# Kernel optimization log

Measured on AMD Instinct MI355X. Metric: run time of the kernel, lower is better.

The kernel has to match this reference:

```python
import jax, jax.numpy as jnp
import numpy as np

T = 4096  # input sequence length; H = T - 16 after convs+pool


def setup_inputs() -> dict:
    key = jax.random.key(0)
    ks = jax.random.split(key, 20)
    def rn(k, shape, scale=0.05):
        return jax.random.normal(k, shape, dtype=jnp.float32) * scale
    return dict(
        evaluation=rn(ks[0], (T, 128), 1.0),
        template=rn(ks[1], (T, 128), 1.0),
        conv1_w=rn(ks[2], (16, 1, 5, 5)),  conv1_b=rn(ks[3], (16,)),
        conv2_w=rn(ks[4], (32, 16, 5, 5)), conv2_b=rn(ks[5], (32,)),
        conv3_w=rn(ks[6], (64, 32, 5, 5)), conv3_b=rn(ks[7], (64,)),
        lin1_w=rn(ks[8], (64, 3712)),      lin1_b=rn(ks[9], (64,)),
        gru_wih=rn(ks[10], (192, 64)),     gru_whh=rn(ks[11], (192, 64)),
        gru_bih=rn(ks[12], (192,)),        gru_bhh=rn(ks[13], (192,)),
        attn_w=rn(ks[14], (1, 64)),        attn_b=rn(ks[15], (1,)),
        lin3_w=rn(ks[16], (128, 64)),      lin3_b=rn(ks[17], (128,)),
        cls_w=rn(ks[18], (2, 128)),        cls_b=rn(ks[19], (2,)),
    )


def _conv(x, w, b):
    y = jax.lax.conv_general_dilated(x, w, (1, 1), 'VALID',
                                     dimension_numbers=('NCHW', 'OIHW', 'NCHW'))
    return y + b[None, :, None, None]


def _encode(x, c1w, c1b, c2w, c2b, c3w, c3b, l1w, l1b, wih, whh, bih, bhh):
    # x: (T, 128) -> (1, 1, T, 128); no activations between convs (as in source)
    x = x.reshape(1, 1, T, 128)
    x = _conv(x, c1w, c1b)   # (1,16,T-4,124)
    x = _conv(x, c2w, c2b)   # (1,32,T-8,120)
    x = _conv(x, c3w, c3b)   # (1,64,T-12,116)
    x = jax.lax.reduce_window(x, -jnp.inf, jax.lax.max,
                              (1, 1, 5, 2), (1, 1, 1, 2), 'VALID')  # (1,64,H,58)
    H = x.shape[2]
    # faithful raw reshape (channel-major flatten), same as torch.reshape
    x = x.reshape(H, 3712)
    x = x @ l1w.T + l1b      # (H, 64)
    # GRU (torch gate order r,z,n), h0 = 0; input gates precomputed
    gi = x @ wih.T + bih     # (H, 192)
    def step(h, gi_t):
        gh = whh @ h + bhh
        ir, iz, inn = jnp.split(gi_t, 3)
        hr, hz, hn = jnp.split(gh, 3)
        r = jax.nn.sigmoid(ir + hr)
        z = jax.nn.sigmoid(iz + hz)
        n = jnp.tanh(inn + r * hn)
        h_new = (1.0 - z) * n + z * h
        return h_new, h_new
    _, out = jax.lax.scan(step, jnp.zeros((64,), dtype=x.dtype), gi)
    return out               # (H, 64)


def reference(evaluation, template, conv1_w, conv1_b, conv2_w, conv2_b,
              conv3_w, conv3_b, lin1_w, lin1_b, gru_wih, gru_whh, gru_bih,
              gru_bhh, attn_w, attn_b, lin3_w, lin3_b, cls_w, cls_b):
    enc = lambda x: _encode(x, conv1_w, conv1_b, conv2_w, conv2_b, conv3_w,
                            conv3_b, lin1_w, lin1_b, gru_wih, gru_whh,
                            gru_bih, gru_bhh)
    e = enc(evaluation)      # (H, 64)
    t = enc(template)        # (H, 64)
    # alignment: aw[m,n] = <e_m, t_n>, softmax over dim 0 (m)
    aw = jax.nn.softmax(e @ t.T, axis=0)      # (H, H)
    t_prim = aw @ t                            # (H, 64)
    distance = jnp.abs(t_prim - e)             # (H, 64)
    attn = jax.nn.softmax((e @ attn_w.T + attn_b).ravel(), axis=0)  # (H,)
    # NOTE: source loops n over distance.size(dim=1)==64, i.e. only the first
    # 64 rows of distance / first 64 attention weights are used (replicated).
    D = distance.shape[1]
    representation = distance[:D].T @ attn[:D]  # (64,)
    out = jax.nn.relu(representation)
    out = jax.nn.relu(out @ lin3_w.T + lin3_b)
    return out @ cls_w.T + cls_b               # (2,)
```

## Files before the change

### kernel.cpp

```cpp
#include <hip/hip_runtime.h>
#include <hip/hip_fp16.h>

constexpr int T_IN = 4096, W_IN = 128;
constexpr int H1 = 4092, W1 = 124, C1 = 16;
constexpr int H2 = 4088, W2 = 120, C2 = 32;
constexpr int H3 = 4084, W3 = 116, C3 = 64;
constexpr int HP = 4080, WPW = 58;
constexpr int KF = 3712;

typedef float f32x16 __attribute__((ext_vector_type(16)));
typedef _Float16 f16x16 __attribute__((ext_vector_type(16)));
typedef _Float16 half2_t __attribute__((ext_vector_type(2)));

static __device__ __forceinline__ half2_t u2h(unsigned int u) {
    half2_t h; __builtin_memcpy(&h, &u, 4); return h;
}

#define LOAD25(SRC, W) \
    float p00=(SRC)[0],        p01=(SRC)[1],        p02=(SRC)[2],        p03=(SRC)[3],        p04=(SRC)[4]; \
    float p10=(SRC)[(W)],      p11=(SRC)[(W)+1],    p12=(SRC)[(W)+2],    p13=(SRC)[(W)+3],    p14=(SRC)[(W)+4]; \
    float p20=(SRC)[2*(W)],    p21=(SRC)[2*(W)+1],  p22=(SRC)[2*(W)+2],  p23=(SRC)[2*(W)+3],  p24=(SRC)[2*(W)+4]; \
    float p30=(SRC)[3*(W)],    p31=(SRC)[3*(W)+1],  p32=(SRC)[3*(W)+2],  p33=(SRC)[3*(W)+3],  p34=(SRC)[3*(W)+4]; \
    float p40=(SRC)[4*(W)],    p41=(SRC)[4*(W)+1],  p42=(SRC)[4*(W)+2],  p43=(SRC)[4*(W)+3],  p44=(SRC)[4*(W)+4];

#define TAPS25(T) \
    T(p00, 0)  T(p01, 1)  T(p02, 2)  T(p03, 3)  T(p04, 4) \
    T(p10, 5)  T(p11, 6)  T(p12, 7)  T(p13, 8)  T(p14, 9) \
    T(p20,10)  T(p21,11)  T(p22,12)  T(p23,13)  T(p24,14) \
    T(p30,15)  T(p31,16)  T(p32,17)  T(p33,18)  T(p34,19) \
    T(p40,20)  T(p41,21)  T(p42,22)  T(p43,23)  T(p44,24)

#define KSTEP16(PK, WPTR) do { \
    const float4* w4_ = (const float4*)(WPTR); \
    float4 wA_ = w4_[0], wB_ = w4_[1], wC_ = w4_[2], wD_ = w4_[3]; \
    a0.x = fmaf((PK), wA_.x, a0.x); a0.y = fmaf((PK), wA_.y, a0.y); \
    a0.z = fmaf((PK), wA_.z, a0.z); a0.w = fmaf((PK), wA_.w, a0.w); \
    a1.x = fmaf((PK), wB_.x, a1.x); a1.y = fmaf((PK), wB_.y, a1.y); \
    a1.z = fmaf((PK), wB_.z, a1.z); a1.w = fmaf((PK), wB_.w, a1.w); \
    a2.x = fmaf((PK), wC_.x, a2.x); a2.y = fmaf((PK), wC_.y, a2.y); \
    a2.z = fmaf((PK), wC_.z, a2.z); a2.w = fmaf((PK), wC_.w, a2.w); \
    a3.x = fmaf((PK), wD_.x, a3.x); a3.y = fmaf((PK), wD_.y, a3.y); \
    a3.z = fmaf((PK), wD_.z, a3.z); a3.w = fmaf((PK), wD_.w, a3.w); \
} while (0)

#define LOAD25H(SRC, W) \
    _Float16 q00=(_Float16)(SRC)[0],      q01=(_Float16)(SRC)[1],      q02=(_Float16)(SRC)[2],      q03=(_Float16)(SRC)[3],      q04=(_Float16)(SRC)[4]; \
    _Float16 q10=(_Float16)(SRC)[(W)],    q11=(_Float16)(SRC)[(W)+1],  q12=(_Float16)(SRC)[(W)+2],  q13=(_Float16)(SRC)[(W)+3],  q14=(_Float16)(SRC)[(W)+4]; \
    _Float16 q20=(_Float16)(SRC)[2*(W)],  q21=(_Float16)(SRC)[2*(W)+1],q22=(_Float16)(SRC)[2*(W)+2],q23=(_Float16)(SRC)[2*(W)+3],q24=(_Float16)(SRC)[2*(W)+4]; \
    _Float16 q30=(_Float16)(SRC)[3*(W)],  q31=(_Float16)(SRC)[3*(W)+1],q32=(_Float16)(SRC)[3*(W)+2],q33=(_Float16)(SRC)[3*(W)+3],q34=(_Float16)(SRC)[3*(W)+4]; \
    _Float16 q40=(_Float16)(SRC)[4*(W)],  q41=(_Float16)(SRC)[4*(W)+1],q42=(_Float16)(SRC)[4*(W)+2],q43=(_Float16)(SRC)[4*(W)+3],q44=(_Float16)(SRC)[4*(W)+4];

#define MKPAIRS() \
    half2_t P0, P1, P2, P3, P4, P5, P6, P7, P8, P9, P10, P11, P12; \
    P0[0]=q00; P0[1]=q01;  P1[0]=q02; P1[1]=q03;  P2[0]=q04; P2[1]=q10; \
    P3[0]=q11; P3[1]=q12;  P4[0]=q13; P4[1]=q14;  P5[0]=q20; P5[1]=q21; \
    P6[0]=q22; P6[1]=q23;  P7[0]=q24; P7[1]=q30;  P8[0]=q31; P8[1]=q32; \
    P9[0]=q33; P9[1]=q34;  P10[0]=q40; P10[1]=q41; P11[0]=q42; P11[1]=q43; \
    P12[0]=q44; P12[1]=(_Float16)0.f;

#define DSTEP16(PH, WPTR) do { \
    const half2_t* wv_ = (const half2_t*)(WPTR); \
    a0.x = __builtin_amdgcn_fdot2((PH), wv_[0],  a0.x, false); \
    a0.y = __builtin_amdgcn_fdot2((PH), wv_[1],  a0.y, false); \
    a0.z = __builtin_amdgcn_fdot2((PH), wv_[2],  a0.z, false); \
    a0.w = __builtin_amdgcn_fdot2((PH), wv_[3],  a0.w, false); \
    a1.x = __builtin_amdgcn_fdot2((PH), wv_[4],  a1.x, false); \
    a1.y = __builtin_amdgcn_fdot2((PH), wv_[5],  a1.y, false); \
    a1.z = __builtin_amdgcn_fdot2((PH), wv_[6],  a1.z, false); \
    a1.w = __builtin_amdgcn_fdot2((PH), wv_[7],  a1.w, false); \
    a2.x = __builtin_amdgcn_fdot2((PH), wv_[8],  a2.x, false); \
    a2.y = __builtin_amdgcn_fdot2((PH), wv_[9],  a2.y, false); \
    a2.z = __builtin_amdgcn_fdot2((PH), wv_[10], a2.z, false); \
    a2.w = __builtin_amdgcn_fdot2((PH), wv_[11], a2.w, false); \
    a3.x = __builtin_amdgcn_fdot2((PH), wv_[12], a3.x, false); \
    a3.y = __builtin_amdgcn_fdot2((PH), wv_[13], a3.y, false); \
    a3.z = __builtin_amdgcn_fdot2((PH), wv_[14], a3.z, false); \
    a3.w = __builtin_amdgcn_fdot2((PH), wv_[15], a3.w, false); \
} while (0)

#define PAIRS13(D, CI) \
    D(P0,  ((CI)*13+ 0)) D(P1,  ((CI)*13+ 1)) D(P2,  ((CI)*13+ 2)) \
    D(P3,  ((CI)*13+ 3)) D(P4,  ((CI)*13+ 4)) D(P5,  ((CI)*13+ 5)) \
    D(P6,  ((CI)*13+ 6)) D(P7,  ((CI)*13+ 7)) D(P8,  ((CI)*13+ 8)) \
    D(P9,  ((CI)*13+ 9)) D(P10, ((CI)*13+10)) D(P11, ((CI)*13+11)) \
    D(P12, ((CI)*13+12))

__global__ __launch_bounds__(256, 2) void conv1_k(const float* __restrict__ x,
        const float* __restrict__ wp, const float* __restrict__ b,
        __half* __restrict__ out) {
    int pos = blockIdx.x * 256 + threadIdx.x;
    if (pos >= H1 * W1) return;
    int h = pos / W1, wi = pos - h * W1;
    const float* src = x + h * W_IN + wi;
    const float4* b4 = (const float4*)b;
    float4 a0 = b4[0], a1 = b4[1], a2 = b4[2], a3 = b4[3];
    LOAD25(src, W_IN);
#define T1(P, K) KSTEP16(P, wp + (K) * 16);
    TAPS25(T1)
#undef T1
#pragma unroll
    for (int i = 0; i < 4; i++) {
        float4 v = (i == 0) ? a0 : (i == 1) ? a1 : (i == 2) ? a2 : a3;
        out[(size_t)(i * 4 + 0) * (H1 * W1) + pos] = __float2half(v.x);
        out[(size_t)(i * 4 + 1) * (H1 * W1) + pos] = __float2half(v.y);
        out[(size_t)(i * 4 + 2) * (H1 * W1) + pos] = __float2half(v.z);
        out[(size_t)(i * 4 + 3) * (H1 * W1) + pos] = __float2half(v.w);
    }
}

__global__ __launch_bounds__(256, 2) void conv2_k(const __half* __restrict__ in,
        const _Float16* __restrict__ wp2, const float* __restrict__ b,
        __half* __restrict__ out) {
    int pos = blockIdx.y * 256 + threadIdx.x;
    if (pos >= H2 * W2) return;
    int co0 = blockIdx.x * 16;
    int h = pos / W2, wi = pos - h * W2;
    const float4* b4 = (const float4*)(b + co0);
    float4 a0 = b4[0], a1 = b4[1], a2 = b4[2], a3 = b4[3];
#pragma unroll 1
    for (int ci = 0; ci < C1; ci++) {
        const __half* src = in + (size_t)ci * (H1 * W1) + h * W1 + wi;
        LOAD25H(src, W1);
        MKPAIRS();
#define D2(PH, QI) DSTEP16(PH, wp2 + ((size_t)(QI) * C2 + co0) * 2);
        PAIRS13(D2, ci)
#undef D2
    }
#pragma unroll
    for (int i = 0; i < 4; i++) {
        float4 v = (i == 0) ? a0 : (i == 1) ? a1 : (i == 2) ? a2 : a3;
        out[(size_t)(co0 + i * 4 + 0) * (H2 * W2) + pos] = __float2half(v.x);
        out[(size_t)(co0 + i * 4 + 1) * (H2 * W2) + pos] = __float2half(v.y);
        out[(size_t)(co0 + i * 4 + 2) * (H2 * W2) + pos] = __float2half(v.z);
        out[(size_t)(co0 + i * 4 + 3) * (H2 * W2) + pos] = __float2half(v.w);
    }
}

__global__ __launch_bounds__(256, 2) void conv3_k(const __half* __restrict__ in,
        const _Float16* __restrict__ wp2, const float* __restrict__ b,
        __half* __restrict__ out) {
    int pos = blockIdx.y * 256 + threadIdx.x;
    if (pos >= H3 * W3) return;
    int co0 = blockIdx.x * 16;
    int h = pos / W3, wi = pos - h * W3;
    const float4* b4 = (const float4*)(b + co0);
    float4 a0 = b4[0], a1 = b4[1], a2 = b4[2], a3 = b4[3];
#pragma unroll 1
    for (int ci = 0; ci < C2; ci++) {
        const __half* src = in + (size_t)ci * (H2 * W2) + h * W2 + wi;
        LOAD25H(src, W2);
        MKPAIRS();
#define D3(PH, QI) DSTEP16(PH, wp2 + ((size_t)(QI) * C3 + co0) * 2);
        PAIRS13(D3, ci)
#undef D3
    }
#pragma unroll
    for (int i = 0; i < 4; i++) {
        float4 v = (i == 0) ? a0 : (i == 1) ? a1 : (i == 2) ? a2 : a3;
        out[(size_t)(co0 + i * 4 + 0) * (H3 * W3) + pos] = __float2half(v.x);
        out[(size_t)(co0 + i * 4 + 1) * (H3 * W3) + pos] = __float2half(v.y);
        out[(size_t)(co0 + i * 4 + 2) * (H3 * W3) + pos] = __float2half(v.z);
        out[(size_t)(co0 + i * 4 + 3) * (H3 * W3) + pos] = __float2half(v.w);
    }
}

__global__ __launch_bounds__(256) void pool_k(const __half* __restrict__ in,
        _Float16* __restrict__ out) {
    int idx = blockIdx.x * 256 + threadIdx.x;
    if (idx >= C3 * HP * WPW) return;
    int w = idx % WPW; int rest = idx / WPW; int h = rest % HP; int c = rest / HP;
    const __half* base = in + (size_t)c * (H3 * W3) + (size_t)h * W3 + 2 * w;
    float m = -1e30f;
#pragma unroll
    for (int i = 0; i < 5; i++)
#pragma unroll
        for (int j = 0; j < 2; j++)
            m = fmaxf(m, __half2float(base[(size_t)i * W3 + j]));
    out[idx] = (_Float16)m;
}

__global__ __launch_bounds__(256, 2) void lin1_k(const _Float16* __restrict__ X,
        const _Float16* __restrict__ Wt2, float* __restrict__ L) {
    __shared__ unsigned int Xs[32][68];
    int tid = threadIdx.x;
    int j = tid & 63, mg = tid >> 6;
    int m0 = blockIdx.x * 64;
    int c0 = blockIdx.y * 15;
    int c1 = (c0 + 15 < 58) ? c0 + 15 : 58;
    float4 la0 = {0.f,0.f,0.f,0.f}, la1 = la0, la2 = la0, la3 = la0;
    for (int cc = c0; cc < c1; cc++) {
        int k0 = cc * 64, kp0 = cc * 32;
        __syncthreads();
#pragma unroll
        for (int t = 0; t < 8; t++) {
            int idx = tid + t * 256;
            int mm = idx >> 5, kk = idx & 31;
            int m = m0 + mm;
            unsigned int v = 0;
            if (m < HP) v = *(const unsigned int*)(X + (size_t)m * KF + k0 + 2 * kk);
            Xs[kk][mm] = v;
        }
        __syncthreads();
#pragma unroll 4
        for (int kk = 0; kk < 32; kk++) {
            unsigned int wvu = *(const unsigned int*)(Wt2 + ((size_t)(kp0 + kk) * 64 + j) * 2);
            half2_t wv = u2h(wvu);
            const uint4* xr = (const uint4*)&Xs[kk][mg * 16];
            uint4 x0 = xr[0], x1 = xr[1], x2 = xr[2], x3 = xr[3];
            la0.x = __builtin_amdgcn_fdot2(u2h(x0.x), wv, la0.x, false);
            la0.y = __builtin_amdgcn_fdot2(u2h(x0.y), wv, la0.y, false);
            la0.z = __builtin_amdgcn_fdot2(u2h(x0.z), wv, la0.z, false);
            la0.w = __builtin_amdgcn_fdot2(u2h(x0.w), wv, la0.w, false);
            la1.x = __builtin_amdgcn_fdot2(u2h(x1.x), wv, la1.x, false);
            la1.y = __builtin_amdgcn_fdot2(u2h(x1.y), wv, la1.y, false);
            la1.z = __builtin_amdgcn_fdot2(u2h(x1.z), wv, la1.z, false);
            la1.w = __builtin_amdgcn_fdot2(u2h(x1.w), wv, la1.w, false);
            la2.x = __builtin_amdgcn_fdot2(u2h(x2.x), wv, la2.x, false);
            la2.y = __builtin_amdgcn_fdot2(u2h(x2.y), wv, la2.y, false);
            la2.z = __builtin_amdgcn_fdot2(u2h(x2.z), wv, la2.z, false);
            la2.w = __builtin_amdgcn_fdot2(u2h(x2.w), wv, la2.w, false);
            la3.x = __builtin_amdgcn_fdot2(u2h(x3.x), wv, la3.x, false);
            la3.y = __builtin_amdgcn_fdot2(u2h(x3.y), wv, la3.y, false);
            la3.z = __builtin_amdgcn_fdot2(u2h(x3.z), wv, la3.z, false);
            la3.w = __builtin_amdgcn_fdot2(u2h(x3.w), wv, la3.w, false);
        }
    }
    int mb = m0 + mg * 16;
#define LATOM(C, OFF) { int m = mb + (OFF); if (m < HP) atomicAdd(&L[(size_t)m * 64 + j], (C)); }
    LATOM(la0.x, 0)  LATOM(la0.y, 1)  LATOM(la0.z, 2)  LATOM(la0.w, 3)
    LATOM(la1.x, 4)  LATOM(la1.y, 5)  LATOM(la1.z, 6)  LATOM(la1.w, 7)
    LATOM(la2.x, 8)  LATOM(la2.y, 9)  LATOM(la2.z, 10) LATOM(la2.w, 11)
    LATOM(la3.x, 12) LATOM(la3.y, 13) LATOM(la3.z, 14) LATOM(la3.w, 15)
#undef LATOM
}

__global__ __launch_bounds__(192) void gi_k(const float* __restrict__ L,
        const float* __restrict__ wiht, const float* __restrict__ bc,
        float* __restrict__ gi) {
    __shared__ alignas(16) float Ls[8][64];
    int m0 = blockIdx.x * 8, g = threadIdx.x;
    for (int idx = g; idx < 512; idx += 192) {
        int r = idx >> 6, k = idx & 63;
        Ls[r][k] = L[(size_t)(m0 + r) * 64 + k];
    }
    __syncthreads();
    float bcv = bc[g];
#pragma unroll 1
    for (int r = 0; r < 8; r++) {
        float acc = bcv;
#pragma unroll
        for (int k = 0; k < 64; k++) acc = fmaf(Ls[r][k], wiht[k * 192 + g], acc);
        gi[(size_t)(m0 + r) * 192 + g] = acc;
    }
}

__global__ __launch_bounds__(192, 1) void gru_k(const float* __restrict__ gi0,
        const float* __restrict__ gi1, const _Float16* __restrict__ whh_h,
        const float* __restrict__ bhh, float* __restrict__ e,
        float* __restrict__ t) {
    const float* gi = blockIdx.x ? gi1 : gi0;
    float* out = blockIdx.x ? t : e;
    const int g = threadIdx.x;
    const f16x16* wp = (const f16x16*)(whh_h + (size_t)g * 64);
    f16x16 w0 = wp[0], w1 = wp[1], w2 = wp[2], w3 = wp[3];
    float bh = bhh[g];
    __shared__ alignas(64) _Float16 hs[64];
    __shared__ float Ax[192];
    const f16x16* hsv = (const f16x16*)hs;
    float h = 0.f;
    if (g < 64) hs[g] = (_Float16)0.f;
    __syncthreads();
    float p0 = 0.f, p1 = 0.f, p2 = 0.f;
    if (g < 64) { p0 = gi[g]; p1 = gi[64 + g]; p2 = gi[128 + g]; }
#define LGKM_BARRIER() do { \
    asm volatile("s_waitcnt lgkmcnt(0)" ::: "memory"); \
    __builtin_amdgcn_s_barrier(); \
    asm volatile("" ::: "memory"); \
} while (0)
#define DOT8(W, H, ACC) _Pragma("unroll") \
    for (int i_ = 0; i_ < 8; i_++) { \
        half2_t wa_; wa_[0] = (W)[2*i_]; wa_[1] = (W)[2*i_+1]; \
        half2_t ha_; ha_[0] = (H)[2*i_]; ha_[1] = (H)[2*i_+1]; \
        ACC = __builtin_amdgcn_fdot2(wa_, ha_, ACC, false); \
    }
#pragma unroll 1
    for (int m = 0; m < HP; m++) {
        f16x16 hv0 = hsv[0], hv1 = hsv[1], hv2 = hsv[2], hv3 = hsv[3];
        float c0 = p0, c1 = p1, c2 = p2;
        if (g < 64 && m + 1 < HP) {
            const float* gp = gi + (size_t)(m + 1) * 192;
            p0 = gp[g]; p1 = gp[64 + g]; p2 = gp[128 + g];
        }
        float a0 = 0.f, a1 = 0.f, a2 = 0.f, a3 = 0.f;
        DOT8(w0, hv0, a0)
        DOT8(w1, hv1, a1)
        DOT8(w2, hv2, a2)
        DOT8(w3, hv3, a3)
        float a = (a0 + a1) + (a2 + a3) + bh;
        Ax[g] = a;
        LGKM_BARRIER();
        if (g < 64) {
            float az = Ax[64 + g], an = Ax[128 + g];
            float rg = 1.f / (1.f + __expf(-(c0 + a)));
            float zg = 1.f / (1.f + __expf(-(c1 + az)));
            float pre = c2 + rg * an;
            float ex = __expf(2.f * pre);
            float nn = 1.f - 2.f / (ex + 1.f);
            h = (1.f - zg) * nn + zg * h;
            hs[g] = (_Float16)h;
            out[(size_t)m * 64 + g] = h;
        }
        LGKM_BARRIER();
    }
#undef DOT8
#undef LGKM_BARRIER
}

__global__ __launch_bounds__(256) void astat_k(const float* __restrict__ e,
        const float* __restrict__ t, float* __restrict__ pM,
        float* __restrict__ pZ) {
    __shared__ alignas(16) float Ts[64][68];
    __shared__ float Ms[4][64], Zs[4][64];
    int tid = threadIdx.x;
    int nl = tid & 63, ms = tid >> 6;
    int n0 = blockIdx.x * 64;
#pragma unroll
    for (int i = 0; i < 16; i++) {
        int idx = tid + i * 256;
        int rr = idx >> 6, kk = idx & 63;
        int n = n0 + rr;
        Ts[rr][kk] = (n < HP) ? t[(size_t)n * 64 + kk] : 0.f;
    }
    __syncthreads();
    float M = -1e30f, Z = 0.f;
    int m0 = blockIdx.y * 510;
    const float4* Trow = (const float4*)&Ts[nl][0];
    for (int m = m0 + ms; m < m0 + 510; m += 4) {
        const float4* er = (const float4*)(e + (size_t)m * 64);
        float a0 = 0, a1 = 0, a2 = 0, a3 = 0;
#pragma unroll
        for (int i = 0; i < 16; i++) {
            float4 evv = er[i], tv = Trow[i];
            a0 = fmaf(evv.x, tv.x, a0); a1 = fmaf(evv.y, tv.y, a1);
            a2 = fmaf(evv.z, tv.z, a2); a3 = fmaf(evv.w, tv.w, a3);
        }
        float s = (a0 + a1) + (a2 + a3);
        float nM = fmaxf(M, s);
        Z = Z * __expf(M - nM) + __expf(s - nM);
        M = nM;
    }
    Ms[ms][nl] = M; Zs[ms][nl] = Z;
    __syncthreads();
    if (ms == 0) {
#pragma unroll
        for (int i = 1; i < 4; i++) {
            float m2 = Ms[i][nl], z2 = Zs[i][nl];
            float nM = fmaxf(M, m2);
            Z = Z * __expf(M - nM) + z2 * __expf(m2 - nM);
            M = nM;
        }
        int n = n0 + nl;
        if (n < HP) { pM[(size_t)blockIdx.y * HP + n] = M; pZ[(size_t)blockIdx.y * HP + n] = Z; }
    }
}

__global__ __launch_bounds__(256) void attnlog_k(const float* __restrict__ e,
        const float* __restrict__ aw, const float* __restrict__ ab,
        float* __restrict__ alog) {
    int m = blockIdx.x * 256 + threadIdx.x;
    if (m >= HP) return;
    float acc = ab[0];
    const float4* er = (const float4*)(e + (size_t)m * 64);
    const float4* ar = (const float4*)aw;
#pragma unroll
    for (int i = 0; i < 16; i++) {
        float4 evv = er[i], av = ar[i];
        acc += evv.x * av.x + evv.y * av.y + evv.z * av.z + evv.w * av.w;
    }
    alog[m] = acc;
}

__global__ __launch_bounds__(256) void reduce_k(const float* __restrict__ pM,
        const float* __restrict__ pZ, float* __restrict__ Mn,
        float* __restrict__ Zn, const float* __restrict__ alog,
        float* __restrict__ scal) {
    int tid = threadIdx.x;
    if (blockIdx.x < 16) {
        int n = blockIdx.x * 256 + tid;
        if (n >= HP) return;
        float M = pM[n], Z = pZ[n];
#pragma unroll
        for (int y = 1; y < 8; y++) {
            float m2 = pM[(size_t)y * HP + n], z2 = pZ[(size_t)y * HP + n];
            float nM = fmaxf(M, m2);
            Z = Z * __expf(M - nM) + z2 * __expf(m2 - nM);
            M = nM;
        }
        Mn[n] = M; Zn[n] = Z;
    } else {
        __shared__ float red[256];
        float m = -1e30f;
        for (int i = tid; i < HP; i += 256) m = fmaxf(m, alog[i]);
        red[tid] = m; __syncthreads();
        for (int s = 128; s > 0; s >>= 1) {
            if (tid < s) red[tid] = fmaxf(red[tid], red[tid + s]);
            __syncthreads();
        }
        float Ma = red[0]; __syncthreads();
        float z = 0.f;
        for (int i = tid; i < HP; i += 256) z += __expf(alog[i] - Ma);
        red[tid] = z; __syncthreads();
        for (int s = 128; s > 0; s >>= 1) {
            if (tid < s) red[tid] += red[tid + s];
            __syncthreads();
        }
        if (tid == 0) { scal[0] = Ma; scal[1] = red[0]; }
    }
}

__global__ __launch_bounds__(256) void wmat_k(const float* __restrict__ e,
        const float* __restrict__ t, const float* __restrict__ Mn,
        const float* __restrict__ Zn, float* __restrict__ Wm) {
    __shared__ alignas(16) float Es[64][68];
    int tid = threadIdx.x;
#pragma unroll
    for (int i = 0; i < 16; i++) {
        int idx = tid + i * 256;
        int rr = idx >> 6, kk = idx & 63;
        Es[rr][kk] = e[(size_t)rr * 64 + kk];
    }
    __syncthreads();
    int n = blockIdx.x * 256 + tid;
    if (n >= HP) return;
    float tn[64];
    const float4* tr = (const float4*)(t + (size_t)n * 64);
    float4* tn4 = (float4*)tn;
#pragma unroll
    for (int i = 0; i < 16; i++) tn4[i] = tr[i];
    float mM = Mn[n], iZ = 1.f / Zn[n];
#pragma unroll 1
    for (int m = 0; m < 64; m++) {
        const float4* Er = (const float4*)&Es[m][0];
        float a0 = 0, a1 = 0, a2 = 0, a3 = 0;
#pragma unroll
        for (int i = 0; i < 16; i++) {
            float4 evv = Er[i], tv = tn4[i];
            a0 = fmaf(evv.x, tv.x, a0); a1 = fmaf(evv.y, tv.y, a1);
            a2 = fmaf(evv.z, tv.z, a2); a3 = fmaf(evv.w, tv.w, a3);
        }
        float s = (a0 + a1) + (a2 + a3);
        Wm[(size_t)m * HP + n] = __expf(s - mM) * iZ;
    }
}

__global__ __launch_bounds__(256) void tprim_k(const float* __restrict__ Wm,
        const float* __restrict__ t, float* __restrict__ tp) {
    __shared__ float Ws[64][64];
    __shared__ float Ts[64][64];
    int tid = threadIdx.x;
    int n0 = blockIdx.x * 64;
#pragma unroll
    for (int i = 0; i < 16; i++) {
        int idx = tid + i * 256;
        int r = idx >> 6, c = idx & 63;
        Ws[r][c] = (n0 + c < HP) ? Wm[(size_t)r * HP + n0 + c] : 0.f;
        Ts[r][c] = (n0 + r < HP) ? t[(size_t)(n0 + r) * 64 + c] : 0.f;
    }
    __syncthreads();
    int d = tid & 63, mg = tid >> 6;
    float acc[16];
#pragma unroll
    for (int i = 0; i < 16; i++) acc[i] = 0.f;
    for (int k = 0; k < 64; k++) {
        float tv = Ts[k][d];
#pragma unroll
        for (int mm = 0; mm < 16; mm++) acc[mm] = fmaf(Ws[mg * 16 + mm][k], tv, acc[mm]);
    }
#pragma unroll
    for (int mm = 0; mm < 16; mm++)
        atomicAdd(&tp[(size_t)(mg * 16 + mm) * 64 + d], acc[mm]);
}

__global__ __launch_bounds__(256) void final_k(const float* __restrict__ tp,
        const float* __restrict__ e, const float* __restrict__ alog,
        const float* __restrict__ scal, const float* __restrict__ l3w,
        const float* __restrict__ l3b, const float* __restrict__ cw,
        const float* __restrict__ cb, float* __restrict__ out) {
    __shared__ float r1[64], hid[128];
    int tid = threadIdx.x;
    float Ma = scal[0], iZa = 1.f / scal[1];
    if (tid < 64) {
        float acc = 0.f;
        for (int m = 0; m < 64; m++) {
            float a = __expf(alog[m] - Ma) * iZa;
            acc += fabsf(tp[m * 64 + tid] - e[m * 64 + tid]) * a;
        }
        r1[tid] = fmaxf(acc, 0.f);
    }
    __syncthreads();
    if (tid < 128) {
        float acc = l3b[tid];
        for (int d = 0; d < 64; d++) acc = fmaf(r1[d], l3w[tid * 64 + d], acc);
        hid[tid] = fmaxf(acc, 0.f);
    }
    __syncthreads();
    if (tid < 2) {
        float acc = cb[tid];
        for (int j = 0; j < 128; j++) acc = fmaf(hid[j], cw[tid * 128 + j], acc);
        out[tid] = acc;
    }
}

__global__ __launch_bounds__(256) void pack_l1w2_k(const float* __restrict__ w,
        _Float16* __restrict__ wt2) {
    int idx = blockIdx.x * 256 + threadIdx.x;
    if (idx >= (KF / 2) * 64) return;
    int kk = idx >> 6, j = idx & 63;
    wt2[(size_t)idx * 2 + 0] = (_Float16)w[(size_t)j * KF + 2 * kk];
    wt2[(size_t)idx * 2 + 1] = (_Float16)w[(size_t)j * KF + 2 * kk + 1];
}
__global__ __launch_bounds__(256) void pack_w1_k(const float* __restrict__ w,
        float* __restrict__ wp) {
    int idx = blockIdx.x * 256 + threadIdx.x;
    if (idx >= 400) return;
    int k = idx >> 4, co = idx & 15;
    wp[idx] = w[co * 25 + k];
}
__global__ __launch_bounds__(256) void pack_w2p_k(const float* __restrict__ w,
        _Float16* __restrict__ wp2) {
    int idx = blockIdx.x * 256 + threadIdx.x;
    if (idx >= 16 * 13 * 32) return;
    int co = idx & 31; int rest = idx >> 5;
    int q = rest % 13, ci = rest / 13;
    int t0 = 2 * q, t1 = 2 * q + 1;
    float v0 = (t0 < 25) ? w[co * 400 + ci * 25 + t0] : 0.f;
    float v1 = (t1 < 25) ? w[co * 400 + ci * 25 + t1] : 0.f;
    wp2[(size_t)idx * 2 + 0] = (_Float16)v0;
    wp2[(size_t)idx * 2 + 1] = (_Float16)v1;
}
__global__ __launch_bounds__(256) void pack_w3p_k(const float* __restrict__ w,
        _Float16* __restrict__ wp2) {
    int idx = blockIdx.x * 256 + threadIdx.x;
    if (idx >= 32 * 13 * 64) return;
    int co = idx & 63; int rest = idx >> 6;
    int q = rest % 13, ci = rest / 13;
    int t0 = 2 * q, t1 = 2 * q + 1;
    float v0 = (t0 < 25) ? w[co * 800 + ci * 25 + t0] : 0.f;
    float v1 = (t1 < 25) ? w[co * 800 + ci * 25 + t1] : 0.f;
    wp2[(size_t)idx * 2 + 0] = (_Float16)v0;
    wp2[(size_t)idx * 2 + 1] = (_Float16)v1;
}
__global__ __launch_bounds__(256) void pack_wih_k(const float* __restrict__ wih,
        const float* __restrict__ bih, const float* __restrict__ l1b,
        const float* __restrict__ whh, float* __restrict__ wiht,
        float* __restrict__ bc, _Float16* __restrict__ whh_h) {
    int idx = blockIdx.x * 256 + threadIdx.x;
    if (idx < 12288) {
        int g = idx % 192, k = idx / 192;
        wiht[idx] = wih[g * 64 + k];
        whh_h[idx] = (_Float16)whh[idx];
    }
    if (idx < 192) {
        float acc = bih[idx];
#pragma unroll
        for (int k = 0; k < 64; k++) acc = fmaf(wih[idx * 64 + k], l1b[k], acc);
        bc[idx] = acc;
    }
}

extern "C" void kernel_launch(void* const* d_in, const int* in_sizes, int n_in,
                              void* d_out, int out_size, void* d_ws, size_t ws_size,
                              hipStream_t stream) {
    const float* ev    = (const float*)d_in[0];
    const float* tmpl  = (const float*)d_in[1];
    const float* w1    = (const float*)d_in[2];
    const float* b1    = (const float*)d_in[3];
    const float* w2    = (const float*)d_in[4];
    const float* b2    = (const float*)d_in[5];
    const float* w3    = (const float*)d_in[6];
    const float* b3    = (const float*)d_in[7];
    const float* l1w   = (const float*)d_in[8];
    const float* l1b   = (const float*)d_in[9];
    const float* wih   = (const float*)d_in[10];
    const float* whh   = (const float*)d_in[11];
    const float* bih   = (const float*)d_in[12];
    const float* bhh   = (const float*)d_in[13];
    const float* aw    = (const float*)d_in[14];
    const float* ab    = (const float*)d_in[15];
    const float* l3w   = (const float*)d_in[16];
    const float* l3b   = (const float*)d_in[17];
    const float* cw    = (const float*)d_in[18];
    const float* cb    = (const float*)d_in[19];
    float* out = (float*)d_out;
    (void)in_sizes; (void)n_in; (void)out_size;

    char* ws = (char*)d_ws;
    size_t off = 0;
    auto alloc = [&](size_t bytes) -> char* {
        char* p = ws + off;
        off += (bytes + 255) & ~(size_t)255;
        return p;
    };
    size_t szA = (size_t)C3 * H3 * W3 * 2;
    char*  A    = alloc(szA);
    char*  B    = alloc((size_t)C2 * H2 * W2 * 2);
    _Float16* P16 = (_Float16*)alloc((size_t)HP * KF * 2);
    _Float16* Wt2 = (_Float16*)alloc((size_t)KF * 64 * 2);
    float* w1p  = (float*)alloc(400 * 4);
    _Float16* w2p2 = (_Float16*)alloc(16 * 13 * 32 * 2 * 2);
    _Float16* w3p2 = (_Float16*)alloc(32 * 13 * 64 * 2 * 2);
    float* wiht = (float*)alloc(12288 * 4);
    _Float16* whhh = (_Float16*)alloc(12288 * 2);
    float* bc   = (float*)alloc(256 * 4);
    float* L    = (float*)alloc((size_t)HP * 64 * 4);
    float* gi0  = (float*)alloc((size_t)HP * 192 * 4);
    float* gi1  = (float*)alloc((size_t)HP * 192 * 4);
    float* ebuf = (float*)alloc((size_t)HP * 64 * 4);
    float* tbuf = (float*)alloc((size_t)HP * 64 * 4);
    float* pM   = (float*)alloc((size_t)8 * HP * 4);
    float* pZ   = (float*)alloc((size_t)8 * HP * 4);
    float* Mn   = (float*)alloc(HP * 4);
    float* Zn   = (float*)alloc(HP * 4);
    float* Wm   = (float*)alloc((size_t)64 * HP * 4);
    float* alog = (float*)alloc(HP * 4);
    float* tpm  = (float*)alloc(64 * 64 * 4);
    float* scal = (float*)alloc(256);
    if (off > ws_size) return;

    pack_l1w2_k<<<dim3(((KF / 2) * 64 + 255) / 256), dim3(256), 0, stream>>>(l1w, Wt2);
    pack_w1_k<<<dim3(2), dim3(256), 0, stream>>>(w1, w1p);
    pack_w2p_k<<<dim3((16 * 13 * 32 + 255) / 256), dim3(256), 0, stream>>>(w2, w2p2);
    pack_w3p_k<<<dim3((32 * 13 * 64 + 255) / 256), dim3(256), 0, stream>>>(w3, w3p2);
    pack_wih_k<<<dim3(48), dim3(256), 0, stream>>>(wih, bih, l1b, whh, wiht, bc, whhh);

    for (int bsel = 0; bsel < 2; bsel++) {
        const float* xin = bsel ? tmpl : ev;
        float* gib = bsel ? gi1 : gi0;
        conv1_k<<<dim3((H1 * W1 + 255) / 256), dim3(256), 0, stream>>>(xin, w1p, b1, (__half*)A);
        conv2_k<<<dim3(2, (H2 * W2 + 255) / 256), dim3(256), 0, stream>>>((const __half*)A, w2p2, b2, (__half*)B);
        conv3_k<<<dim3(4, (H3 * W3 + 255) / 256), dim3(256), 0, stream>>>((const __half*)B, w3p2, b3, (__half*)A);
        pool_k<<<dim3((C3 * HP * WPW + 255) / 256), dim3(256), 0, stream>>>((const __half*)A, P16);
        hipMemsetAsync(L, 0, (size_t)HP * 64 * 4, stream);
        lin1_k<<<dim3(64, 4), dim3(256), 0, stream>>>(P16, Wt2, L);
        gi_k<<<dim3(HP / 8), dim3(192), 0, stream>>>(L, wiht, bc, gib);
    }
    gru_k<<<dim3(2), dim3(192), 0, stream>>>(gi0, gi1, whhh, bhh, ebuf, tbuf);
    astat_k<<<dim3(64, 8), dim3(256), 0, stream>>>(ebuf, tbuf, pM, pZ);
    attnlog_k<<<dim3(16), dim3(256), 0, stream>>>(ebuf, aw, ab, alog);
    reduce_k<<<dim3(17), dim3(256), 0, stream>>>(pM, pZ, Mn, Zn, alog, scal);
    wmat_k<<<dim3(16), dim3(256), 0, stream>>>(ebuf, tbuf, Mn, Zn, Wm);
    hipMemsetAsync(tpm, 0, 64 * 64 * 4, stream);
    tprim_k<<<dim3(64), dim3(256), 0, stream>>>(Wm, tbuf, tpm);
    final_k<<<dim3(1), dim3(256), 0, stream>>>(tpm, ebuf, alog, scal, l3w, l3b, cw, cb, out);
}
```

Baseline: 3.400 ms.

## Compute two adjacent output columns per thread in conv2/conv3 with packed half2 loads

Each thread in conv2 and conv3 now produces two horizontally adjacent output pixels, so it keeps two accumulator sets that share the same weight loads. Input rows are read as 32-bit words and reshuffled into half2 pairs with shifts, replacing the 25 scalar fp16 loads and the per-element pair packing. The weights are repacked row-wise into 15 pairs per input channel instead of 13, and outputs are written as half2. This halves thread count and weight traffic per output at the cost of more registers per thread, which may reduce occupancy, and a few extra zero-padded dot products.

```diff
diff --git a/kernel.cpp b/kernel.cpp
--- a/kernel.cpp
+++ b/kernel.cpp
@@ -43,22 +43,7 @@
     a3.z = fmaf((PK), wD_.z, a3.z); a3.w = fmaf((PK), wD_.w, a3.w); \
 } while (0)
 
-#define LOAD25H(SRC, W) \
-    _Float16 q00=(_Float16)(SRC)[0],      q01=(_Float16)(SRC)[1],      q02=(_Float16)(SRC)[2],      q03=(_Float16)(SRC)[3],      q04=(_Float16)(SRC)[4]; \
-    _Float16 q10=(_Float16)(SRC)[(W)],    q11=(_Float16)(SRC)[(W)+1],  q12=(_Float16)(SRC)[(W)+2],  q13=(_Float16)(SRC)[(W)+3],  q14=(_Float16)(SRC)[(W)+4]; \
-    _Float16 q20=(_Float16)(SRC)[2*(W)],  q21=(_Float16)(SRC)[2*(W)+1],q22=(_Float16)(SRC)[2*(W)+2],q23=(_Float16)(SRC)[2*(W)+3],q24=(_Float16)(SRC)[2*(W)+4]; \
-    _Float16 q30=(_Float16)(SRC)[3*(W)],  q31=(_Float16)(SRC)[3*(W)+1],q32=(_Float16)(SRC)[3*(W)+2],q33=(_Float16)(SRC)[3*(W)+3],q34=(_Float16)(SRC)[3*(W)+4]; \
-    _Float16 q40=(_Float16)(SRC)[4*(W)],  q41=(_Float16)(SRC)[4*(W)+1],q42=(_Float16)(SRC)[4*(W)+2],q43=(_Float16)(SRC)[4*(W)+3],q44=(_Float16)(SRC)[4*(W)+4];
-
-#define MKPAIRS() \
-    half2_t P0, P1, P2, P3, P4, P5, P6, P7, P8, P9, P10, P11, P12; \
-    P0[0]=q00; P0[1]=q01;  P1[0]=q02; P1[1]=q03;  P2[0]=q04; P2[1]=q10; \
-    P3[0]=q11; P3[1]=q12;  P4[0]=q13; P4[1]=q14;  P5[0]=q20; P5[1]=q21; \
-    P6[0]=q22; P6[1]=q23;  P7[0]=q24; P7[1]=q30;  P8[0]=q31; P8[1]=q32; \
-    P9[0]=q33; P9[1]=q34;  P10[0]=q40; P10[1]=q41; P11[0]=q42; P11[1]=q43; \
-    P12[0]=q44; P12[1]=(_Float16)0.f;
-
-#define DSTEP16(PH, WPTR) do { \
+#define DSTEP16A(PH, WPTR) do { \
     const half2_t* wv_ = (const half2_t*)(WPTR); \
     a0.x = __builtin_amdgcn_fdot2((PH), wv_[0],  a0.x, false); \
     a0.y = __builtin_amdgcn_fdot2((PH), wv_[1],  a0.y, false); \
@@ -78,12 +63,25 @@
     a3.w = __builtin_amdgcn_fdot2((PH), wv_[15], a3.w, false); \
 } while (0)
 
-#define PAIRS13(D, CI) \
-    D(P0,  ((CI)*13+ 0)) D(P1,  ((CI)*13+ 1)) D(P2,  ((CI)*13+ 2)) \
-    D(P3,  ((CI)*13+ 3)) D(P4,  ((CI)*13+ 4)) D(P5,  ((CI)*13+ 5)) \
-    D(P6,  ((CI)*13+ 6)) D(P7,  ((CI)*13+ 7)) D(P8,  ((CI)*13+ 8)) \
-    D(P9,  ((CI)*13+ 9)) D(P10, ((CI)*13+10)) D(P11, ((CI)*13+11)) \
-    D(P12, ((CI)*13+12))
+#define DSTEP16B(PH, WPTR) do { \
+    const half2_t* wv_ = (const half2_t*)(WPTR); \
+    b0.x = __builtin_amdgcn_fdot2((PH), wv_[0],  b0.x, false); \
+    b0.y = __builtin_amdgcn_fdot2((PH), wv_[1],  b0.y, false); \
+    b0.z = __builtin_amdgcn_fdot2((PH), wv_[2],  b0.z, false); \
+    b0.w = __builtin_amdgcn_fdot2((PH), wv_[3],  b0.w, false); \
+    b1.x = __builtin_amdgcn_fdot2((PH), wv_[4],  b1.x, false); \
+    b1.y = __builtin_amdgcn_fdot2((PH), wv_[5],  b1.y, false); \
+    b1.z = __builtin_amdgcn_fdot2((PH), wv_[6],  b1.z, false); \
+    b1.w = __builtin_amdgcn_fdot2((PH), wv_[7],  b1.w, false); \
+    b2.x = __builtin_amdgcn_fdot2((PH), wv_[8],  b2.x, false); \
+    b2.y = __builtin_amdgcn_fdot2((PH), wv_[9],  b2.y, false); \
+    b2.z = __builtin_amdgcn_fdot2((PH), wv_[10], b2.z, false); \
+    b2.w = __builtin_amdgcn_fdot2((PH), wv_[11], b2.w, false); \
+    b3.x = __builtin_amdgcn_fdot2((PH), wv_[12], b3.x, false); \
+    b3.y = __builtin_amdgcn_fdot2((PH), wv_[13], b3.y, false); \
+    b3.z = __builtin_amdgcn_fdot2((PH), wv_[14], b3.z, false); \
+    b3.w = __builtin_amdgcn_fdot2((PH), wv_[15], b3.w, false); \
+} while (0)
 
 __global__ __launch_bounds__(256, 2) void conv1_k(const float* __restrict__ x,
         const float* __restrict__ wp, const float* __restrict__ b,
@@ -111,57 +109,81 @@
 __global__ __launch_bounds__(256, 2) void conv2_k(const __half* __restrict__ in,
         const _Float16* __restrict__ wp2, const float* __restrict__ b,
         __half* __restrict__ out) {
-    int pos = blockIdx.y * 256 + threadIdx.x;
-    if (pos >= H2 * W2) return;
+    constexpr int WH = W2 / 2;
+    int pid = blockIdx.y * 256 + threadIdx.x;
+    if (pid >= H2 * WH) return;
     int co0 = blockIdx.x * 16;
-    int h = pos / W2, wi = pos - h * W2;
+    int h = pid / WH, wi = 2 * (pid - h * WH);
     const float4* b4 = (const float4*)(b + co0);
     float4 a0 = b4[0], a1 = b4[1], a2 = b4[2], a3 = b4[3];
+    float4 b0 = a0, b1 = a1, b2 = a2, b3 = a3;
 #pragma unroll 1
     for (int ci = 0; ci < C1; ci++) {
-        const __half* src = in + (size_t)ci * (H1 * W1) + h * W1 + wi;
-        LOAD25H(src, W1);
-        MKPAIRS();
-#define D2(PH, QI) DSTEP16(PH, wp2 + ((size_t)(QI) * C2 + co0) * 2);
-        PAIRS13(D2, ci)
-#undef D2
-    }
-#pragma unroll
-    for (int i = 0; i < 4; i++) {
-        float4 v = (i == 0) ? a0 : (i == 1) ? a1 : (i == 2) ? a2 : a3;
-        out[(size_t)(co0 + i * 4 + 0) * (H2 * W2) + pos] = __float2half(v.x);
-        out[(size_t)(co0 + i * 4 + 1) * (H2 * W2) + pos] = __float2half(v.y);
-        out[(size_t)(co0 + i * 4 + 2) * (H2 * W2) + pos] = __float2half(v.z);
-        out[(size_t)(co0 + i * 4 + 3) * (H2 * W2) + pos] = __float2half(v.w);
-    }
+        const __half* base = in + (size_t)ci * (H1 * W1) + (size_t)h * W1 + wi;
+#pragma unroll
+        for (int i = 0; i < 5; i++) {
+            const unsigned int* rp = (const unsigned int*)(base + (size_t)i * W1);
+            unsigned int u0 = rp[0], u1 = rp[1], u2 = rp[2];
+            unsigned int bp0 = (u0 >> 16) | (u1 << 16);
+            unsigned int bp1 = (u1 >> 16) | (u2 << 16);
+            int q = ci * 15 + i * 3;
+            const _Float16* w0p = wp2 + ((size_t)(q + 0) * C2 + co0) * 2;
+            const _Float16* w1p = wp2 + ((size_t)(q + 1) * C2 + co0) * 2;
+            const _Float16* w2p = wp2 + ((size_t)(q + 2) * C2 + co0) * 2;
+            DSTEP16A(u2h(u0), w0p);  DSTEP16B(u2h(bp0), w0p);
+            DSTEP16A(u2h(u1), w1p);  DSTEP16B(u2h(bp1), w1p);
+            DSTEP16A(u2h(u2 & 0xffffu), w2p);
+            DSTEP16B(u2h(u2 >> 16), w2p);
+        }
+    }
+    int pos = h * W2 + wi;
+#define ST2(C, AV, BV) { half2_t hv; hv[0] = (_Float16)(AV); hv[1] = (_Float16)(BV); \
+    *(half2_t*)(out + (size_t)(co0 + (C)) * (H2 * W2) + pos) = hv; }
+    ST2(0, a0.x, b0.x)  ST2(1, a0.y, b0.y)  ST2(2, a0.z, b0.z)  ST2(3, a0.w, b0.w)
+    ST2(4, a1.x, b1.x)  ST2(5, a1.y, b1.y)  ST2(6, a1.z, b1.z)  ST2(7, a1.w, b1.w)
+    ST2(8, a2.x, b2.x)  ST2(9, a2.y, b2.y)  ST2(10, a2.z, b2.z) ST2(11, a2.w, b2.w)
+    ST2(12, a3.x, b3.x) ST2(13, a3.y, b3.y) ST2(14, a3.z, b3.z) ST2(15, a3.w, b3.w)
+#undef ST2
 }
 
 __global__ __launch_bounds__(256, 2) void conv3_k(const __half* __restrict__ in,
         const _Float16* __restrict__ wp2, const float* __restrict__ b,
         __half* __restrict__ out) {
-    int pos = blockIdx.y * 256 + threadIdx.x;
-    if (pos >= H3 * W3) return;
+    constexpr int WH = W3 / 2;
+    int pid = blockIdx.y * 256 + threadIdx.x;
+    if (pid >= H3 * WH) return;
     int co0 = blockIdx.x * 16;
-    int h = pos / W3, wi = pos - h * W3;
+    int h = pid / WH, wi = 2 * (pid - h * WH);
     const float4* b4 = (const float4*)(b + co0);
     float4 a0 = b4[0], a1 = b4[1], a2 = b4[2], a3 = b4[3];
+    float4 b0 = a0, b1 = a1, b2 = a2, b3 = a3;
 #pragma unroll 1
     for (int ci = 0; ci < C2; ci++) {
-        const __half* src = in + (size_t)ci * (H2 * W2) + h * W2 + wi;
-        LOAD25H(src, W2);
-        MKPAIRS();
-#define D3(PH, QI) DSTEP16(PH, wp2 + ((size_t)(QI) * C3 + co0) * 2);
-        PAIRS13(D3, ci)
-#undef D3
-    }
-#pragma unroll
-    for (int i = 0; i < 4; i++) {
-        float4 v = (i == 0) ? a0 : (i == 1) ? a1 : (i == 2) ? a2 : a3;
-        out[(size_t)(co0 + i * 4 + 0) * (H3 * W3) + pos] = __float2half(v.x);
-        out[(size_t)(co0 + i * 4 + 1) * (H3 * W3) + pos] = __float2half(v.y);
-        out[(size_t)(co0 + i * 4 + 2) * (H3 * W3) + pos] = __float2half(v.z);
-        out[(size_t)(co0 + i * 4 + 3) * (H3 * W3) + pos] = __float2half(v.w);
-    }
+        const __half* base = in + (size_t)ci * (H2 * W2) + (size_t)h * W2 + wi;
+#pragma unroll
+        for (int i = 0; i < 5; i++) {
+            const unsigned int* rp = (const unsigned int*)(base + (size_t)i * W2);
+            unsigned int u0 = rp[0], u1 = rp[1], u2 = rp[2];
+            unsigned int bp0 = (u0 >> 16) | (u1 << 16);
+            unsigned int bp1 = (u1 >> 16) | (u2 << 16);
+            int q = ci * 15 + i * 3;
+            const _Float16* w0p = wp2 + ((size_t)(q + 0) * C3 + co0) * 2;
+            const _Float16* w1p = wp2 + ((size_t)(q + 1) * C3 + co0) * 2;
+            const _Float16* w2p = wp2 + ((size_t)(q + 2) * C3 + co0) * 2;
+            DSTEP16A(u2h(u0), w0p);  DSTEP16B(u2h(bp0), w0p);
+            DSTEP16A(u2h(u1), w1p);  DSTEP16B(u2h(bp1), w1p);
+            DSTEP16A(u2h(u2 & 0xffffu), w2p);
+            DSTEP16B(u2h(u2 >> 16), w2p);
+        }
+    }
+    int pos = h * W3 + wi;
+#define ST3(C, AV, BV) { half2_t hv; hv[0] = (_Float16)(AV); hv[1] = (_Float16)(BV); \
+    *(half2_t*)(out + (size_t)(co0 + (C)) * (H3 * W3) + pos) = hv; }
+    ST3(0, a0.x, b0.x)  ST3(1, a0.y, b0.y)  ST3(2, a0.z, b0.z)  ST3(3, a0.w, b0.w)
+    ST3(4, a1.x, b1.x)  ST3(5, a1.y, b1.y)  ST3(6, a1.z, b1.z)  ST3(7, a1.w, b1.w)
+    ST3(8, a2.x, b2.x)  ST3(9, a2.y, b2.y)  ST3(10, a2.z, b2.z) ST3(11, a2.w, b2.w)
+    ST3(12, a3.x, b3.x) ST3(13, a3.y, b3.y) ST3(14, a3.z, b3.z) ST3(15, a3.w, b3.w)
+#undef ST3
 }
 
 __global__ __launch_bounds__(256) void pool_k(const __half* __restrict__ in,
@@ -529,24 +551,26 @@
 __global__ __launch_bounds__(256) void pack_w2p_k(const float* __restrict__ w,
         _Float16* __restrict__ wp2) {
     int idx = blockIdx.x * 256 + threadIdx.x;
-    if (idx >= 16 * 13 * 32) return;
+    if (idx >= 16 * 15 * 32) return;
     int co = idx & 31; int rest = idx >> 5;
-    int q = rest % 13, ci = rest / 13;
-    int t0 = 2 * q, t1 = 2 * q + 1;
-    float v0 = (t0 < 25) ? w[co * 400 + ci * 25 + t0] : 0.f;
-    float v1 = (t1 < 25) ? w[co * 400 + ci * 25 + t1] : 0.f;
+    int q = rest % 15, ci = rest / 15;
+    int row = q / 3, r = q % 3;
+    int t0 = row * 5 + 2 * r;
+    float v0 = w[co * 400 + ci * 25 + t0];
+    float v1 = (r < 2) ? w[co * 400 + ci * 25 + t0 + 1] : 0.f;
     wp2[(size_t)idx * 2 + 0] = (_Float16)v0;
     wp2[(size_t)idx * 2 + 1] = (_Float16)v1;
 }
 __global__ __launch_bounds__(256) void pack_w3p_k(const float* __restrict__ w,
         _Float16* __restrict__ wp2) {
     int idx = blockIdx.x * 256 + threadIdx.x;
-    if (idx >= 32 * 13 * 64) return;
+    if (idx >= 32 * 15 * 64) return;
     int co = idx & 63; int rest = idx >> 6;
-    int q = rest % 13, ci = rest / 13;
-    int t0 = 2 * q, t1 = 2 * q + 1;
-    float v0 = (t0 < 25) ? w[co * 800 + ci * 25 + t0] : 0.f;
-    float v1 = (t1 < 25) ? w[co * 800 + ci * 25 + t1] : 0.f;
+    int q = rest % 15, ci = rest / 15;
+    int row = q / 3, r = q % 3;
+    int t0 = row * 5 + 2 * r;
+    float v0 = w[co * 800 + ci * 25 + t0];
+    float v1 = (r < 2) ? w[co * 800 + ci * 25 + t0 + 1] : 0.f;
     wp2[(size_t)idx * 2 + 0] = (_Float16)v0;
     wp2[(size_t)idx * 2 + 1] = (_Float16)v1;
 }
@@ -607,8 +631,8 @@
     _Float16* P16 = (_Float16*)alloc((size_t)HP * KF * 2);
     _Float16* Wt2 = (_Float16*)alloc((size_t)KF * 64 * 2);
     float* w1p  = (float*)alloc(400 * 4);
-    _Float16* w2p2 = (_Float16*)alloc(16 * 13 * 32 * 2 * 2);
-    _Float16* w3p2 = (_Float16*)alloc(32 * 13 * 64 * 2 * 2);
+    _Float16* w2p2 = (_Float16*)alloc(16 * 15 * 32 * 2 * 2);
+    _Float16* w3p2 = (_Float16*)alloc(32 * 15 * 64 * 2 * 2);
     float* wiht = (float*)alloc(12288 * 4);
     _Float16* whhh = (_Float16*)alloc(12288 * 2);
     float* bc   = (float*)alloc(256 * 4);
@@ -629,16 +653,16 @@
 
     pack_l1w2_k<<<dim3(((KF / 2) * 64 + 255) / 256), dim3(256), 0, stream>>>(l1w, Wt2);
     pack_w1_k<<<dim3(2), dim3(256), 0, stream>>>(w1, w1p);
-    pack_w2p_k<<<dim3((16 * 13 * 32 + 255) / 256), dim3(256), 0, stream>>>(w2, w2p2);
-    pack_w3p_k<<<dim3((32 * 13 * 64 + 255) / 256), dim3(256), 0, stream>>>(w3, w3p2);
+    pack_w2p_k<<<dim3((16 * 15 * 32 + 255) / 256), dim3(256), 0, stream>>>(w2, w2p2);
+    pack_w3p_k<<<dim3((32 * 15 * 64 + 255) / 256), dim3(256), 0, stream>>>(w3, w3p2);
     pack_wih_k<<<dim3(48), dim3(256), 0, stream>>>(wih, bih, l1b, whh, wiht, bc, whhh);
 
     for (int bsel = 0; bsel < 2; bsel++) {
         const float* xin = bsel ? tmpl : ev;
         float* gib = bsel ? gi1 : gi0;
         conv1_k<<<dim3((H1 * W1 + 255) / 256), dim3(256), 0, stream>>>(xin, w1p, b1, (__half*)A);
-        conv2_k<<<dim3(2, (H2 * W2 + 255) / 256), dim3(256), 0, stream>>>((const __half*)A, w2p2, b2, (__half*)B);
-        conv3_k<<<dim3(4, (H3 * W3 + 255) / 256), dim3(256), 0, stream>>>((const __half*)B, w3p2, b3, (__half*)A);
+        conv2_k<<<dim3(2, (H2 * (W2 / 2) + 255) / 256), dim3(256), 0, stream>>>((const __half*)A, w2p2, b2, (__half*)B);
+        conv3_k<<<dim3(4, (H3 * (W3 / 2) + 255) / 256), dim3(256), 0, stream>>>((const __half*)B, w3p2, b3, (__half*)A);
         pool_k<<<dim3((C3 * HP * WPW + 255) / 256), dim3(256), 0, stream>>>((const __half*)A, P16);
         hipMemsetAsync(L, 0, (size_t)HP * 64 * 4, stream);
         lin1_k<<<dim3(64, 4), dim3(256), 0, stream>>>(P16, Wt2, L);
```

Result: slower. 3.529 ms (+3.8%).
